# Kernel optimization log

Measured on AMD Instinct MI355X. Metric: run time of the kernel, lower is better.

## Reference

```python
import jax, jax.numpy as jnp
import numpy as np

B, L, D_MODEL, H = 2, 2048, 1024, 16
HD = D_MODEL // H  # head dim = 64


def setup_inputs() -> dict:
    key = jax.random.key(0)
    ks = jax.random.split(key, 11)
    s = 1.0 / np.sqrt(D_MODEL)
    inp = {
        "Q": jax.random.normal(ks[0], (B, L, D_MODEL), jnp.float32),
        "K": jax.random.normal(ks[1], (B, L, D_MODEL), jnp.float32),
        "V": jax.random.normal(ks[2], (B, L, D_MODEL), jnp.float32),
        "Wq": jax.random.normal(ks[3], (D_MODEL, D_MODEL), jnp.float32) * s,
        "bq": jnp.zeros((D_MODEL,), jnp.float32),
        "Wk": jax.random.normal(ks[4], (D_MODEL, D_MODEL), jnp.float32) * s,
        "bk": jnp.zeros((D_MODEL,), jnp.float32),
        "Wv": jax.random.normal(ks[5], (D_MODEL, D_MODEL), jnp.float32) * s,
        "bv": jnp.zeros((D_MODEL,), jnp.float32),
        "Wo": jax.random.normal(ks[6], (D_MODEL, D_MODEL), jnp.float32) * s,
        "bo": jnp.zeros((D_MODEL,), jnp.float32),
    }
    return inp


def _split_heads(x):
    # [B, L, H*D] -> [B, H, L, D]
    return x.reshape(B, L, H, HD).transpose(0, 2, 1, 3)


def reference(Q, K, V, Wq, bq, Wk, bk, Wv, bv, Wo, bo):
    q = _split_heads(Q @ Wq.T + bq)
    k = _split_heads(K @ Wk.T + bk)
    v = _split_heads(V @ Wv.T + bv)
    scale = 1.0 / jnp.sqrt(jnp.asarray(HD, q.dtype))
    # full [B, H, L, L] score matrix, as in the original bmm->softmax->bmm
    scores = jnp.einsum("bhqd,bhkd->bhqk", q, k) * scale
    attn = jax.nn.softmax(scores, axis=-1)
    o = jnp.einsum("bhqk,bhkd->bhqd", attn, v)
    o = o.transpose(0, 2, 1, 3).reshape(B, L, D_MODEL)  # concat heads
    return o @ Wo.T + bo
```

## Files before the change

kernel.cpp:

```cpp
#include <hip/hip_runtime.h>
#include <math.h>
#include <stdint.h>

typedef __bf16 bf16_t;
typedef __attribute__((ext_vector_type(8))) __bf16 bf16x8;
typedef __attribute__((ext_vector_type(4))) float f32x4;
typedef __attribute__((ext_vector_type(16))) float f32x16;
typedef __attribute__((address_space(1))) unsigned int gu32;
typedef __attribute__((address_space(3))) unsigned int lu32;

#define MFMA16(a, b, c) __builtin_amdgcn_mfma_f32_16x16x32_bf16((a), (b), (c), 0, 0, 0)
#define MFMA32(a, b, c) __builtin_amdgcn_mfma_f32_32x32x16_bf16((a), (b), (c), 0, 0, 0)

__device__ __forceinline__ void gll16(const void* g, void* l) {
    __builtin_amdgcn_global_load_lds((const gu32*)(uintptr_t)g,
                                     (lu32*)(uintptr_t)l, 16, 0, 0);
}

__device__ __forceinline__ bf16x8 ld_frag68(const bf16_t* p) {
    union { bf16x8 v; uint2 u[2]; } r;
    r.u[0] = *(const uint2*)p;
    r.u[1] = *(const uint2*)(p + 4);
    return r.v;
}

__global__ __launch_bounds__(256) void convert_all(
    const float* __restrict__ Q, const float* __restrict__ K, const float* __restrict__ V,
    const float* __restrict__ Wq, const float* __restrict__ Wk, const float* __restrict__ Wv,
    const float* __restrict__ Wo, bf16_t* __restrict__ dst) {
    size_t e0 = (size_t)blockIdx.x * 2048;
    const float* src; size_t off;
    if (e0 < 4194304)       { src = Q;  off = e0; }
    else if (e0 < 8388608)  { src = K;  off = e0 - 4194304; }
    else if (e0 < 12582912) { src = V;  off = e0 - 8388608; }
    else if (e0 < 13631488) { src = Wq; off = e0 - 12582912; }
    else if (e0 < 14680064) { src = Wk; off = e0 - 13631488; }
    else if (e0 < 15728640) { src = Wv; off = e0 - 14680064; }
    else                    { src = Wo; off = e0 - 15728640; }
#pragma unroll
    for (int p = 0; p < 2; ++p) {
        int t = p * 1024 + threadIdx.x * 4;
        float4 v = *(const float4*)(src + off + t);
        union { ushort4 u; bf16_t h[4]; } pk;
        pk.h[0] = (bf16_t)v.x; pk.h[1] = (bf16_t)v.y;
        pk.h[2] = (bf16_t)v.z; pk.h[3] = (bf16_t)v.w;
        *(ushort4*)(dst + e0 + t) = pk.u;
    }
}

__global__ __launch_bounds__(256) void qkv_gemm(
    const bf16_t* __restrict__ Qb, const bf16_t* __restrict__ Kb, const bf16_t* __restrict__ Vb,
    const bf16_t* __restrict__ Wqb, const bf16_t* __restrict__ Wkb, const bf16_t* __restrict__ Wvb,
    const float* __restrict__ bq, const float* __restrict__ bk, const float* __restrict__ bv,
    bf16_t* __restrict__ qo, bf16_t* __restrict__ ko, bf16_t* __restrict__ vT) {
    constexpr int Kdim = 1024, N = 1024;
    __shared__ __attribute__((aligned(16))) bf16_t As[128 * 64];
    __shared__ __attribute__((aligned(16))) bf16_t Bs[128 * 64];

    const int tid = threadIdx.x, wave = tid >> 6, lane = tid & 63;
    const int z = blockIdx.z;
    const bf16_t* A = (z == 0) ? Qb : (z == 1) ? Kb : Vb;
    const bf16_t* W = (z == 0) ? Wqb : (z == 1) ? Wkb : Wvb;
    const float* bias = (z == 0) ? bq : (z == 1) ? bk : bv;
    const int bm = blockIdx.y * 128, bn = blockIdx.x * 128;
    const int l16 = lane & 15, quad = lane >> 4;
    const int wm = (wave >> 1) * 64, wn = (wave & 1) * 64;
    const int grow = lane >> 3, gcol = (lane & 7) * 8;

    f32x4 acc[4][4] = {};

    for (int k0 = 0; k0 < Kdim; k0 += 64) {
#pragma unroll
        for (int j = 0; j < 4; ++j) {
            int chunk = wave * 4 + j;
            int row = chunk * 8 + grow;
            gll16(A + (size_t)(bm + row) * Kdim + k0 + gcol, As + chunk * 512);
            gll16(W + (size_t)(bn + row) * Kdim + k0 + gcol, Bs + chunk * 512);
        }
        __syncthreads();
#pragma unroll
        for (int ks = 0; ks < 64; ks += 32) {
            bf16x8 af[4], bf[4];
#pragma unroll
            for (int i = 0; i < 4; ++i)
                af[i] = *(const bf16x8*)&As[(wm + i * 16 + l16) * 64 + ks + quad * 8];
#pragma unroll
            for (int i = 0; i < 4; ++i)
                bf[i] = *(const bf16x8*)&Bs[(wn + i * 16 + l16) * 64 + ks + quad * 8];
#pragma unroll
            for (int i = 0; i < 4; ++i)
#pragma unroll
                for (int j = 0; j < 4; ++j)
                    acc[i][j] = MFMA16(af[i], bf[j], acc[i][j]);
        }
        __syncthreads();
    }

    if (z < 2) {
        bf16_t* outp = (z == 0) ? qo : ko;
        const float sc = (z == 0) ? 0.125f : 1.0f;
#pragma unroll
        for (int mi = 0; mi < 4; ++mi)
#pragma unroll
            for (int nj = 0; nj < 4; ++nj) {
                int col = bn + wn + nj * 16 + l16;
                float bv_ = bias[col];
#pragma unroll
                for (int r = 0; r < 4; ++r) {
                    int row = bm + wm + mi * 16 + quad * 4 + r;
                    outp[(size_t)row * N + col] = (bf16_t)((acc[mi][nj][r] + bv_) * sc);
                }
            }
    } else {
#pragma unroll
        for (int mi = 0; mi < 4; ++mi)
#pragma unroll
            for (int nj = 0; nj < 4; ++nj) {
                int col = bn + wn + nj * 16 + l16;
                int h = col >> 6, d = col & 63;
                float bv_ = bias[col];
                int row0 = bm + wm + mi * 16 + quad * 4;
                int bb = row0 >> 11, l = row0 & 2047;
                union { ushort4 u; bf16_t h4[4]; } pk;
#pragma unroll
                for (int r = 0; r < 4; ++r) pk.h4[r] = (bf16_t)(acc[mi][nj][r] + bv_);
                *(ushort4*)&vT[(((size_t)bb * 16 + h) * 64 + d) * 2048 + l] = pk.u;
            }
    }
}

__global__ __launch_bounds__(256) void out_gemm(const bf16_t* __restrict__ A,
                                                const bf16_t* __restrict__ W,
                                                const float* __restrict__ bias,
                                                float* __restrict__ out) {
    constexpr int Kdim = 1024, N = 1024;
    __shared__ __attribute__((aligned(16))) bf16_t As[128 * 64];
    __shared__ __attribute__((aligned(16))) bf16_t Bs[128 * 64];
    const int tid = threadIdx.x, wave = tid >> 6, lane = tid & 63;
    const int bm = blockIdx.y * 128, bn = blockIdx.x * 128;
    const int l16 = lane & 15, quad = lane >> 4;
    const int wm = (wave >> 1) * 64, wn = (wave & 1) * 64;
    const int grow = lane >> 3, gcol = (lane & 7) * 8;
    f32x4 acc[4][4] = {};

    for (int k0 = 0; k0 < Kdim; k0 += 64) {
#pragma unroll
        for (int j = 0; j < 4; ++j) {
            int chunk = wave * 4 + j;
            int row = chunk * 8 + grow;
            gll16(A + (size_t)(bm + row) * Kdim + k0 + gcol, As + chunk * 512);
            gll16(W + (size_t)(bn + row) * Kdim + k0 + gcol, Bs + chunk * 512);
        }
        __syncthreads();
#pragma unroll
        for (int ks = 0; ks < 64; ks += 32) {
            bf16x8 af[4], bf[4];
#pragma unroll
            for (int i = 0; i < 4; ++i)
                af[i] = *(const bf16x8*)&As[(wm + i * 16 + l16) * 64 + ks + quad * 8];
#pragma unroll
            for (int i = 0; i < 4; ++i)
                bf[i] = *(const bf16x8*)&Bs[(wn + i * 16 + l16) * 64 + ks + quad * 8];
#pragma unroll
            for (int i = 0; i < 4; ++i)
#pragma unroll
                for (int j = 0; j < 4; ++j)
                    acc[i][j] = MFMA16(af[i], bf[j], acc[i][j]);
        }
        __syncthreads();
    }
#pragma unroll
    for (int mi = 0; mi < 4; ++mi)
#pragma unroll
        for (int nj = 0; nj < 4; ++nj) {
            int col = bn + wn + nj * 16 + l16;
            float bv_ = bias[col];
#pragma unroll
            for (int r = 0; r < 4; ++r) {
                int row = bm + wm + mi * 16 + quad * 4 + r;
                out[(size_t)row * N + col] = acc[mi][nj][r] + bv_;
            }
        }
}

__global__ __launch_bounds__(256) void attn3(const bf16_t* __restrict__ qo,
                                             const bf16_t* __restrict__ ko,
                                             const bf16_t* __restrict__ vT,
                                             bf16_t* __restrict__ Ob) {
    constexpr int L = 2048, D = 1024, HD = 64, ST = 68;
    __shared__ __attribute__((aligned(16))) bf16_t ksm[64 * ST];
    __shared__ __attribute__((aligned(16))) bf16_t vsm[64 * ST];
    __shared__ __attribute__((aligned(16))) bf16_t psm[4][32 * ST];

    const int tid = threadIdx.x, wave = tid >> 6, lane = tid & 63;
    const int l31 = lane & 31, hi = lane >> 5;
    const int b = blockIdx.y >> 4, h = blockIdx.y & 15;
    const int q0 = blockIdx.x * 128;
    bf16_t* pw = psm[wave];

    const int rloc = tid >> 2, cg = tid & 3;
    const bf16_t* kbase = ko + ((size_t)b * L + rloc) * D + h * HD + cg * 16;
    const bf16_t* vbase = vT + (((size_t)b * 16 + h) * HD + rloc) * L + cg * 16;

    bf16x8 qf[4];
    {
        const bf16_t* qptr = qo + ((size_t)b * L + q0 + wave * 32 + l31) * D + h * HD + hi * 8;
#pragma unroll
        for (int ks = 0; ks < 4; ++ks) qf[ks] = *(const bf16x8*)(qptr + ks * 16);
    }

    f32x16 o0{}, o1{};
    float lp[16];
#pragma unroll
    for (int r = 0; r < 16; ++r) lp[r] = 0.f;

    for (int kt = 0; kt < L / 64; ++kt) {
        const size_t koff = (size_t)(kt * 64) * D;
        const int voff = kt * 64;
        uint4 ka = *(const uint4*)(kbase + koff);
        uint4 kc = *(const uint4*)(kbase + koff + 8);
        uint4 va = *(const uint4*)(vbase + voff);
        uint4 vc = *(const uint4*)(vbase + voff + 8);
        __syncthreads();
        {
            bf16_t* kd = &ksm[rloc * ST + cg * 16];
            bf16_t* vd = &vsm[rloc * ST + cg * 16];
            *(uint2*)(kd + 0)  = make_uint2(ka.x, ka.y);
            *(uint2*)(kd + 4)  = make_uint2(ka.z, ka.w);
            *(uint2*)(kd + 8)  = make_uint2(kc.x, kc.y);
            *(uint2*)(kd + 12) = make_uint2(kc.z, kc.w);
            *(uint2*)(vd + 0)  = make_uint2(va.x, va.y);
            *(uint2*)(vd + 4)  = make_uint2(va.z, va.w);
            *(uint2*)(vd + 8)  = make_uint2(vc.x, vc.y);
            *(uint2*)(vd + 12) = make_uint2(vc.z, vc.w);
        }
        __syncthreads();

        f32x16 s0{}, s1{};
#pragma unroll
        for (int ks = 0; ks < 4; ++ks) {
            bf16x8 b0 = ld_frag68(&ksm[l31 * ST + ks * 16 + hi * 8]);
            bf16x8 b1 = ld_frag68(&ksm[(32 + l31) * ST + ks * 16 + hi * 8]);
            s0 = MFMA32(qf[ks], b0, s0);
            s1 = MFMA32(qf[ks], b1, s1);
        }

#pragma unroll
        for (int r = 0; r < 16; ++r) {
            int row = (r & 3) + 8 * (r >> 2) + 4 * hi;
            float p0 = __expf(s0[r]);
            float p1 = __expf(s1[r]);
            lp[r] += p0 + p1;
            pw[row * ST + l31] = (bf16_t)p0;
            pw[row * ST + 32 + l31] = (bf16_t)p1;
        }

#pragma unroll
        for (int ks = 0; ks < 4; ++ks) {
            bf16x8 a  = ld_frag68(&pw[l31 * ST + ks * 16 + hi * 8]);
            bf16x8 b0 = ld_frag68(&vsm[l31 * ST + ks * 16 + hi * 8]);
            bf16x8 b1 = ld_frag68(&vsm[(32 + l31) * ST + ks * 16 + hi * 8]);
            o0 = MFMA32(a, b0, o0);
            o1 = MFMA32(a, b1, o1);
        }
    }

#pragma unroll
    for (int r = 0; r < 16; ++r) {
        lp[r] += __shfl_xor(lp[r], 1, 64);
        lp[r] += __shfl_xor(lp[r], 2, 64);
        lp[r] += __shfl_xor(lp[r], 4, 64);
        lp[r] += __shfl_xor(lp[r], 8, 64);
        lp[r] += __shfl_xor(lp[r], 16, 64);
    }

#pragma unroll
    for (int r = 0; r < 16; ++r) {
        int row = (r & 3) + 8 * (r >> 2) + 4 * hi;
        float inv = 1.f / lp[r];
        size_t base = ((size_t)b * L + q0 + wave * 32 + row) * D + h * HD;
        Ob[base + l31] = (bf16_t)(o0[r] * inv);
        Ob[base + 32 + l31] = (bf16_t)(o1[r] * inv);
    }
}

extern "C" void kernel_launch(void* const* d_in, const int* in_sizes, int n_in,
                              void* d_out, int out_size, void* d_ws, size_t ws_size,
                              hipStream_t stream) {
    const float* Q  = (const float*)d_in[0];
    const float* Kx = (const float*)d_in[1];
    const float* V  = (const float*)d_in[2];
    const float* Wq = (const float*)d_in[3];
    const float* bq = (const float*)d_in[4];
    const float* Wk = (const float*)d_in[5];
    const float* bk = (const float*)d_in[6];
    const float* Wv = (const float*)d_in[7];
    const float* bv = (const float*)d_in[8];
    const float* Wo = (const float*)d_in[9];
    const float* bo = (const float*)d_in[10];

    bf16_t* ws0 = (bf16_t*)d_ws;
    bf16_t* Qb  = ws0;
    bf16_t* Kb  = ws0 + 4194304;
    bf16_t* Vb  = ws0 + 8388608;
    bf16_t* Wqb = ws0 + 12582912;
    bf16_t* Wkb = ws0 + 13631488;
    bf16_t* Wvb = ws0 + 14680064;
    bf16_t* Wob = ws0 + 15728640;
    bf16_t* vT  = ws0 + 16777216;
    bf16_t* qo = (bf16_t*)d_out;
    bf16_t* ko = qo + 4194304;
    bf16_t* Ob = Qb;

    convert_all<<<8192, 256, 0, stream>>>(Q, Kx, V, Wq, Wk, Wv, Wo, ws0);
    qkv_gemm<<<dim3(8, 32, 3), 256, 0, stream>>>(Qb, Kb, Vb, Wqb, Wkb, Wvb,
                                                 bq, bk, bv, qo, ko, vT);
    attn3<<<dim3(16, 32), 256, 0, stream>>>(qo, ko, vT, Ob);
    out_gemm<<<dim3(8, 32), 256, 0, stream>>>(Ob, Wob, bo, (float*)d_out);
}
```

Before: 260.0 us.

## Double-buffer attention K/V tiles, use exp2 with folded log2e, shrink out_gemm tiles

The attention kernel now double-buffers K and V in shared memory. The next tile's global loads are issued before the current tile's MFMAs and stored afterwards, so each iteration has one barrier instead of two. The Q scale now folds in log2(e), which lets exp2f replace __expf. The output GEMM moves from 128x128 to 64x128 tiles and doubles the grid, giving more blocks for the 256 CUs at the cost of less reuse per block.

```diff
diff --git a/kernel.cpp b/kernel.cpp
--- a/kernel.cpp
+++ b/kernel.cpp
@@ -98,7 +98,7 @@
 
     if (z < 2) {
         bf16_t* outp = (z == 0) ? qo : ko;
-        const float sc = (z == 0) ? 0.125f : 1.0f;
+        const float sc = (z == 0) ? 0.18033688011112042f : 1.0f;
 #pragma unroll
         for (int mi = 0; mi < 4; ++mi)
 #pragma unroll
@@ -134,35 +134,40 @@
                                                 const float* __restrict__ bias,
                                                 float* __restrict__ out) {
     constexpr int Kdim = 1024, N = 1024;
-    __shared__ __attribute__((aligned(16))) bf16_t As[128 * 64];
+    __shared__ __attribute__((aligned(16))) bf16_t As[64 * 64];
     __shared__ __attribute__((aligned(16))) bf16_t Bs[128 * 64];
     const int tid = threadIdx.x, wave = tid >> 6, lane = tid & 63;
-    const int bm = blockIdx.y * 128, bn = blockIdx.x * 128;
+    const int bm = blockIdx.y * 64, bn = blockIdx.x * 128;
     const int l16 = lane & 15, quad = lane >> 4;
-    const int wm = (wave >> 1) * 64, wn = (wave & 1) * 64;
+    const int wm = (wave >> 1) * 32, wn = (wave & 1) * 64;
     const int grow = lane >> 3, gcol = (lane & 7) * 8;
-    f32x4 acc[4][4] = {};
+    f32x4 acc[2][4] = {};
 
     for (int k0 = 0; k0 < Kdim; k0 += 64) {
+#pragma unroll
+        for (int j = 0; j < 2; ++j) {
+            int chunk = wave * 2 + j;
+            int row = chunk * 8 + grow;
+            gll16(A + (size_t)(bm + row) * Kdim + k0 + gcol, As + chunk * 512);
+        }
 #pragma unroll
         for (int j = 0; j < 4; ++j) {
             int chunk = wave * 4 + j;
             int row = chunk * 8 + grow;
-            gll16(A + (size_t)(bm + row) * Kdim + k0 + gcol, As + chunk * 512);
             gll16(W + (size_t)(bn + row) * Kdim + k0 + gcol, Bs + chunk * 512);
         }
         __syncthreads();
 #pragma unroll
         for (int ks = 0; ks < 64; ks += 32) {
-            bf16x8 af[4], bf[4];
-#pragma unroll
-            for (int i = 0; i < 4; ++i)
+            bf16x8 af[2], bf[4];
+#pragma unroll
+            for (int i = 0; i < 2; ++i)
                 af[i] = *(const bf16x8*)&As[(wm + i * 16 + l16) * 64 + ks + quad * 8];
 #pragma unroll
             for (int i = 0; i < 4; ++i)
                 bf[i] = *(const bf16x8*)&Bs[(wn + i * 16 + l16) * 64 + ks + quad * 8];
 #pragma unroll
-            for (int i = 0; i < 4; ++i)
+            for (int i = 0; i < 2; ++i)
 #pragma unroll
                 for (int j = 0; j < 4; ++j)
                     acc[i][j] = MFMA16(af[i], bf[j], acc[i][j]);
@@ -170,7 +175,7 @@
         __syncthreads();
     }
 #pragma unroll
-    for (int mi = 0; mi < 4; ++mi)
+    for (int mi = 0; mi < 2; ++mi)
 #pragma unroll
         for (int nj = 0; nj < 4; ++nj) {
             int col = bn + wn + nj * 16 + l16;
@@ -183,13 +188,13 @@
         }
 }
 
-__global__ __launch_bounds__(256) void attn3(const bf16_t* __restrict__ qo,
+__global__ __launch_bounds__(256) void attn4(const bf16_t* __restrict__ qo,
                                              const bf16_t* __restrict__ ko,
                                              const bf16_t* __restrict__ vT,
                                              bf16_t* __restrict__ Ob) {
-    constexpr int L = 2048, D = 1024, HD = 64, ST = 68;
-    __shared__ __attribute__((aligned(16))) bf16_t ksm[64 * ST];
-    __shared__ __attribute__((aligned(16))) bf16_t vsm[64 * ST];
+    constexpr int L = 2048, D = 1024, ST = 68;
+    __shared__ __attribute__((aligned(16))) bf16_t ksm[2][64 * ST];
+    __shared__ __attribute__((aligned(16))) bf16_t vsm[2][64 * ST];
     __shared__ __attribute__((aligned(16))) bf16_t psm[4][32 * ST];
 
     const int tid = threadIdx.x, wave = tid >> 6, lane = tid & 63;
@@ -199,15 +204,33 @@
     bf16_t* pw = psm[wave];
 
     const int rloc = tid >> 2, cg = tid & 3;
-    const bf16_t* kbase = ko + ((size_t)b * L + rloc) * D + h * HD + cg * 16;
-    const bf16_t* vbase = vT + (((size_t)b * 16 + h) * HD + rloc) * L + cg * 16;
+    const bf16_t* kbase = ko + ((size_t)b * L + rloc) * D + h * 64 + cg * 16;
+    const bf16_t* vbase = vT + (((size_t)b * 16 + h) * 64 + rloc) * L + cg * 16;
 
     bf16x8 qf[4];
     {
-        const bf16_t* qptr = qo + ((size_t)b * L + q0 + wave * 32 + l31) * D + h * HD + hi * 8;
+        const bf16_t* qptr = qo + ((size_t)b * L + q0 + wave * 32 + l31) * D + h * 64 + hi * 8;
 #pragma unroll
         for (int ks = 0; ks < 4; ++ks) qf[ks] = *(const bf16x8*)(qptr + ks * 16);
     }
+
+    uint4 ka = *(const uint4*)(kbase);
+    uint4 kc = *(const uint4*)(kbase + 8);
+    uint4 va = *(const uint4*)(vbase);
+    uint4 vc = *(const uint4*)(vbase + 8);
+    {
+        bf16_t* kd = &ksm[0][rloc * ST + cg * 16];
+        bf16_t* vd = &vsm[0][rloc * ST + cg * 16];
+        *(uint2*)(kd + 0)  = make_uint2(ka.x, ka.y);
+        *(uint2*)(kd + 4)  = make_uint2(ka.z, ka.w);
+        *(uint2*)(kd + 8)  = make_uint2(kc.x, kc.y);
+        *(uint2*)(kd + 12) = make_uint2(kc.z, kc.w);
+        *(uint2*)(vd + 0)  = make_uint2(va.x, va.y);
+        *(uint2*)(vd + 4)  = make_uint2(va.z, va.w);
+        *(uint2*)(vd + 8)  = make_uint2(vc.x, vc.y);
+        *(uint2*)(vd + 12) = make_uint2(vc.z, vc.w);
+    }
+    __syncthreads();
 
     f32x16 o0{}, o1{};
     float lp[16];
@@ -215,16 +238,50 @@
     for (int r = 0; r < 16; ++r) lp[r] = 0.f;
 
     for (int kt = 0; kt < L / 64; ++kt) {
-        const size_t koff = (size_t)(kt * 64) * D;
-        const int voff = kt * 64;
-        uint4 ka = *(const uint4*)(kbase + koff);
-        uint4 kc = *(const uint4*)(kbase + koff + 8);
-        uint4 va = *(const uint4*)(vbase + voff);
-        uint4 vc = *(const uint4*)(vbase + voff + 8);
-        __syncthreads();
-        {
-            bf16_t* kd = &ksm[rloc * ST + cg * 16];
-            bf16_t* vd = &vsm[rloc * ST + cg * 16];
+        const int cur = kt & 1;
+        const bf16_t* km = ksm[cur];
+        const bf16_t* vm = vsm[cur];
+
+        if (kt < L / 64 - 1) {
+            const size_t koff = (size_t)((kt + 1) * 64) * D;
+            const int voff = (kt + 1) * 64;
+            ka = *(const uint4*)(kbase + koff);
+            kc = *(const uint4*)(kbase + koff + 8);
+            va = *(const uint4*)(vbase + voff);
+            vc = *(const uint4*)(vbase + voff + 8);
+        }
+
+        f32x16 s0{}, s1{};
+#pragma unroll
+        for (int ks = 0; ks < 4; ++ks) {
+            bf16x8 b0 = ld_frag68(&km[l31 * ST + ks * 16 + hi * 8]);
+            bf16x8 b1 = ld_frag68(&km[(32 + l31) * ST + ks * 16 + hi * 8]);
+            s0 = MFMA32(qf[ks], b0, s0);
+            s1 = MFMA32(qf[ks], b1, s1);
+        }
+
+#pragma unroll
+        for (int r = 0; r < 16; ++r) {
+            int row = (r & 3) + 8 * (r >> 2) + 4 * hi;
+            float p0 = exp2f(s0[r]);
+            float p1 = exp2f(s1[r]);
+            lp[r] += p0 + p1;
+            pw[row * ST + l31] = (bf16_t)p0;
+            pw[row * ST + 32 + l31] = (bf16_t)p1;
+        }
+
+#pragma unroll
+        for (int ks = 0; ks < 4; ++ks) {
+            bf16x8 a  = ld_frag68(&pw[l31 * ST + ks * 16 + hi * 8]);
+            bf16x8 b0 = ld_frag68(&vm[l31 * ST + ks * 16 + hi * 8]);
+            bf16x8 b1 = ld_frag68(&vm[(32 + l31) * ST + ks * 16 + hi * 8]);
+            o0 = MFMA32(a, b0, o0);
+            o1 = MFMA32(a, b1, o1);
+        }
+
+        if (kt < L / 64 - 1) {
+            bf16_t* kd = &ksm[cur ^ 1][rloc * ST + cg * 16];
+            bf16_t* vd = &vsm[cur ^ 1][rloc * ST + cg * 16];
             *(uint2*)(kd + 0)  = make_uint2(ka.x, ka.y);
             *(uint2*)(kd + 4)  = make_uint2(ka.z, ka.w);
             *(uint2*)(kd + 8)  = make_uint2(kc.x, kc.y);
@@ -235,34 +292,6 @@
             *(uint2*)(vd + 12) = make_uint2(vc.z, vc.w);
         }
         __syncthreads();
-
-        f32x16 s0{}, s1{};
-#pragma unroll
-        for (int ks = 0; ks < 4; ++ks) {
-            bf16x8 b0 = ld_frag68(&ksm[l31 * ST + ks * 16 + hi * 8]);
-            bf16x8 b1 = ld_frag68(&ksm[(32 + l31) * ST + ks * 16 + hi * 8]);
-            s0 = MFMA32(qf[ks], b0, s0);
-            s1 = MFMA32(qf[ks], b1, s1);
-        }
-
-#pragma unroll
-        for (int r = 0; r < 16; ++r) {
-            int row = (r & 3) + 8 * (r >> 2) + 4 * hi;
-            float p0 = __expf(s0[r]);
-            float p1 = __expf(s1[r]);
-            lp[r] += p0 + p1;
-            pw[row * ST + l31] = (bf16_t)p0;
-            pw[row * ST + 32 + l31] = (bf16_t)p1;
-        }
-
-#pragma unroll
-        for (int ks = 0; ks < 4; ++ks) {
-            bf16x8 a  = ld_frag68(&pw[l31 * ST + ks * 16 + hi * 8]);
-            bf16x8 b0 = ld_frag68(&vsm[l31 * ST + ks * 16 + hi * 8]);
-            bf16x8 b1 = ld_frag68(&vsm[(32 + l31) * ST + ks * 16 + hi * 8]);
-            o0 = MFMA32(a, b0, o0);
-            o1 = MFMA32(a, b1, o1);
-        }
     }
 
 #pragma unroll
@@ -278,7 +307,7 @@
     for (int r = 0; r < 16; ++r) {
         int row = (r & 3) + 8 * (r >> 2) + 4 * hi;
         float inv = 1.f / lp[r];
-        size_t base = ((size_t)b * L + q0 + wave * 32 + row) * D + h * HD;
+        size_t base = ((size_t)b * L + q0 + wave * 32 + row) * D + h * 64;
         Ob[base + l31] = (bf16_t)(o0[r] * inv);
         Ob[base + 32 + l31] = (bf16_t)(o1[r] * inv);
     }
@@ -315,6 +344,6 @@
     convert_all<<<8192, 256, 0, stream>>>(Q, Kx, V, Wq, Wk, Wv, Wo, ws0);
     qkv_gemm<<<dim3(8, 32, 3), 256, 0, stream>>>(Qb, Kb, Vb, Wqb, Wkb, Wvb,
                                                  bq, bk, bv, qo, ko, vT);
-    attn3<<<dim3(16, 32), 256, 0, stream>>>(qo, ko, vT, Ob);
-    out_gemm<<<dim3(8, 32), 256, 0, stream>>>(Ob, Wob, bo, (float*)d_out);
-}
+    attn4<<<dim3(16, 32), 256, 0, stream>>>(qo, ko, vT, Ob);
+    out_gemm<<<dim3(8, 64), 256, 0, stream>>>(Ob, Wob, bo, (float*)d_out);
+}
```

Result: slower. 272.6 us (+4.8%).
